# Performance work log

Hardware: AMD Instinct MI355X
Metric: run time of the kernel (lower is better)

Reference implementation:

```python
import jax, jax.numpy as jnp
import numpy as np

L, B, S, D, H, DH, F, W = 4, 4, 1024, 768, 12, 64, 3072, 128
R = 2 * W + 1  # 257 relative positions
EPS = 1e-8


def setup_inputs() -> dict:
    key = jax.random.key(0)
    ks = jax.random.split(key, 12)
    sc = 0.02
    rn = lambda k, shape: (jax.random.normal(k, shape, jnp.float32) * sc)
    return {
        'hidden_states': jax.random.normal(ks[0], (B, S, D), jnp.float32),
        'workspace_states': jax.random.normal(ks[1], (B, 8, D), jnp.float32),
        'attention_mask': jnp.ones((B, S), dtype=bool),
        'wq': rn(ks[2], (L, D, D)),
        'wk': rn(ks[3], (L, D, D)),
        'wv': rn(ks[4], (L, D, D)),
        'pos_q': rn(ks[5], (L, H, DH, R)),
        'pos_k': rn(ks[6], (L, H, DH, R)),
        'wo': rn(ks[7], (L, D, D)),
        'bo': jnp.zeros((L, D), jnp.float32),
        'w1': rn(ks[8], (L, D, F)),
        'b1': jnp.zeros((L, F), jnp.float32),
        'w2': rn(ks[9], (L, F, D)),
        'b2': jnp.zeros((L, D), jnp.float32),
        'ln_g': jnp.ones((L, D), jnp.float32),
        'ln_b': jnp.zeros((L, D), jnp.float32),
    }


def _encoder(hidden_states, workspace_states, attention_mask,
             wq, wk, wv, pos_q, pos_k, wo, bo, w1, b1, w2, b2, ln_g, ln_b):
    mask = attention_mask.astype(bool)
    ii = jnp.arange(S)[:, None]
    jj = jnp.arange(S)[None, :]
    # index = clamp(-(i-j) + w, 0, 2w)  -> relative-position bucket per (i,j)
    rel = jnp.clip(jj - ii + W, 0, 2 * W)            # [S,S] int
    band = jnp.abs(ii - jj) <= W                      # triu(-w) & ~triu(w+1)
    m = band[None, None] & mask[:, None, None, :] & mask[:, None, :, None]
    neg = jnp.finfo(jnp.float32).min
    h = hidden_states
    for l in range(L):
        q = (h @ wq[l]).reshape(B, S, H, DH).transpose(0, 2, 1, 3)  # [B,H,S,d]
        k = (h @ wk[l]).reshape(B, S, H, DH).transpose(0, 2, 1, 3)
        v = (h @ wv[l]).reshape(B, S, H, DH).transpose(0, 2, 1, 3)
        score = jnp.einsum('bhid,bhjd->bhij', q, k)
        qpk = jnp.einsum('bhid,hdr->bhir', q, pos_k[l])  # content-to-position
        kpq = jnp.einsum('bhjd,hdr->bhjr', k, pos_q[l])  # position-to-content
        c2p = qpk[:, :, ii, rel]                          # gather -> [B,H,S,S]
        p2c = jnp.swapaxes(kpq[:, :, ii, rel], -1, -2)    # gather + transpose
        score = score + c2p + p2c + neg * (~m)
        proba = jax.nn.softmax(score, axis=-1)
        ctx = jnp.einsum('bhij,bhjd->bhid', proba, v)
        ctx = ctx.transpose(0, 2, 1, 3).reshape(B, S, D)
        h = h + ctx @ wo[l] + bo[l]
        # shared workspace unit: pass-through (zero hidden update)
        inter = jax.nn.gelu(h @ w1[l] + b1[l], approximate=False)
        h = h + inter @ w2[l] + b2[l]
        mu = jnp.mean(h, axis=-1, keepdims=True)
        var = jnp.var(h, axis=-1, keepdims=True)
        h = (h - mu) / jnp.sqrt(var + EPS) * ln_g[l] + ln_b[l]
    return h


def reference(hidden_states, workspace_states, attention_mask,
              wq, wk, wv, pos_q, pos_k, wo, bo, w1, b1, w2, b2, ln_g, ln_b):
    return _encoder(hidden_states, workspace_states, attention_mask,
                    wq, wk, wv, pos_q, pos_k, wo, bo, w1, b1, w2, b2, ln_g, ln_b)
```

## Files before the change

### kernel.cpp

```cpp
#include <hip/hip_runtime.h>
#include <cstdint>
#include <cstddef>

#define L_ 4
#define B_ 4
#define S_ 1024
#define D_ 768
#define H_ 12
#define DH_ 64
#define F_ 3072
#define W_ 128
#define R_ 257
#define RP2_ 272
#define PTR_ 384

using f32x4 = __attribute__((ext_vector_type(4))) float;
typedef __bf16 bf16x8 __attribute__((ext_vector_type(8)));

__device__ __forceinline__ float bf2f(ushort u) {
  union { uint32_t i; float f; } x; x.i = ((uint32_t)u) << 16; return x.f;
}
__device__ __forceinline__ ushort f2bf(float f) {
  union { float f; uint32_t i; } x; x.f = f;
  uint32_t r = x.i + 0x7FFFu + ((x.i >> 16) & 1u);
  return (ushort)(r >> 16);
}

__global__ __launch_bounds__(256)
void transpose_cvt(const float* __restrict__ in, ushort* __restrict__ out,
                   int K, int N)
{
  __shared__ float tile[32][33];
  int n0 = blockIdx.x * 32, k0 = blockIdx.y * 32;
  int tx = threadIdx.x & 31, ty = threadIdx.x >> 5;
  #pragma unroll
  for (int r = 0; r < 32; r += 8)
    tile[ty + r][tx] = in[(size_t)(k0 + ty + r) * N + n0 + tx];
  __syncthreads();
  #pragma unroll
  for (int r = 0; r < 32; r += 8)
    out[(size_t)(n0 + ty + r) * K + k0 + tx] = f2bf(tile[tx][ty + r]);
}

__global__ __launch_bounds__(256)
void pos_transpose(const float* __restrict__ pos, ushort* __restrict__ posT)
{
  __shared__ float tile[32][33];
  int lh = blockIdx.x;
  int rt = blockIdx.y;
  int dt = blockIdx.z;
  int tx = threadIdx.x & 31, ty = threadIdx.x >> 5;
  const float* src = pos + (size_t)lh * 64 * R_;
  #pragma unroll
  for (int rr = 0; rr < 32; rr += 8) {
    int d = dt * 32 + ty + rr, r = rt * 32 + tx;
    tile[ty + rr][tx] = (r < R_) ? src[(size_t)d * R_ + r] : 0.f;
  }
  __syncthreads();
  ushort* dst = posT + (size_t)lh * PTR_ * 64;
  #pragma unroll
  for (int rr = 0; rr < 32; rr += 8) {
    int r = rt * 32 + ty + rr, d = dt * 32 + tx;
    dst[(size_t)r * 64 + d] = f2bf(tile[tx][ty + rr]);
  }
}

__global__ __launch_bounds__(256)
void init_h(const float* __restrict__ in, float* __restrict__ h,
            ushort* __restrict__ hbf, int n)
{
  int idx = blockIdx.x * 256 + threadIdx.x;
  if (idx < n) { float v = in[idx]; h[idx] = v; hbf[idx] = f2bf(v); }
}

__global__ __launch_bounds__(256)
void copy_out(const float* __restrict__ h, float* __restrict__ out, int n)
{
  int idx = blockIdx.x * 256 + threadIdx.x;
  if (idx < n) out[idx] = h[idx];
}

template<int EPI>
__global__ __launch_bounds__(256)
void gemm_bt(const ushort* __restrict__ A, const ushort* __restrict__ Bt,
             int M, int N, int K, const float* __restrict__ bias,
             float* __restrict__ resid, ushort* __restrict__ outbf)
{
  constexpr int KP = 56;
  __shared__ ushort Asm[128 * KP];
  __shared__ ushort Bsm[128 * KP];
  const int bm = blockIdx.x, bn = blockIdx.y;
  const int tid = threadIdx.x;
  const int lane = tid & 63, wave = tid >> 6;
  const int wm = wave >> 1, wn = wave & 1;
  const int srow = tid >> 2, scol = (tid & 3) * 8;
  const size_t rowA0 = (size_t)bm * 128, rowB0 = (size_t)bn * 128;
  const int fr = lane & 15;
  const int kb = (lane >> 4) * 8;

  f32x4 acc[4][4] = {};

  for (int k0 = 0; k0 < K; k0 += 32) {
    __syncthreads();
    #pragma unroll
    for (int it = 0; it < 2; ++it) {
      int r = srow + it * 64;
      *(uint4*)(&Asm[r * KP + scol]) =
          *(const uint4*)(A + (rowA0 + r) * K + k0 + scol);
      *(uint4*)(&Bsm[r * KP + scol]) =
          *(const uint4*)(Bt + (rowB0 + r) * K + k0 + scol);
    }
    __syncthreads();
    bf16x8 af[4], bfr[4];
    #pragma unroll
    for (int m = 0; m < 4; ++m)
      af[m] = *(const bf16x8*)(&Asm[(wm * 64 + m * 16 + fr) * KP + kb]);
    #pragma unroll
    for (int n = 0; n < 4; ++n)
      bfr[n] = *(const bf16x8*)(&Bsm[(wn * 64 + n * 16 + fr) * KP + kb]);
    #pragma unroll
    for (int m = 0; m < 4; ++m)
      #pragma unroll
      for (int n = 0; n < 4; ++n)
        acc[m][n] = __builtin_amdgcn_mfma_f32_16x16x32_bf16(
            af[m], bfr[n], acc[m][n], 0, 0, 0);
  }

  const int cr = (lane >> 4) * 4, cc = lane & 15;
  #pragma unroll
  for (int m = 0; m < 4; ++m) {
    #pragma unroll
    for (int n = 0; n < 4; ++n) {
      #pragma unroll
      for (int q = 0; q < 4; ++q) {
        size_t row = rowA0 + wm * 64 + m * 16 + cr + q;
        size_t col = rowB0 + wn * 64 + n * 16 + cc;
        float v = acc[m][n][q];
        if constexpr (EPI == 0) {
          outbf[row * N + col] = f2bf(v);
        } else if constexpr (EPI == 1) {
          float x = v + bias[col];
          float g = 0.5f * x * (1.0f + erff(x * 0.70710678118654752f));
          outbf[row * N + col] = f2bf(g);
        } else if constexpr (EPI == 2) {
          float x = v + bias[col] + resid[row * N + col];
          resid[row * N + col] = x;
          outbf[row * N + col] = f2bf(x);
        } else {
          float x = v + bias[col] + resid[row * N + col];
          resid[row * N + col] = x;
        }
      }
    }
  }
}

__global__ __launch_bounds__(256)
void pos_mfma(const ushort* __restrict__ qkv,
              const ushort* __restrict__ posTq, const ushort* __restrict__ posTk,
              ushort* __restrict__ qpk, ushort* __restrict__ kpq)
{
  __shared__ ushort Asm[128 * 64];
  __shared__ ushort Bsm[128 * 64];
  const int bm = blockIdx.x, bn = blockIdx.y, z = blockIdx.z;
  const int h = z >> 1, which = z & 1;
  const ushort* A  = qkv + (which ? 768 : 0) + h * 64;
  const ushort* Bt = (which ? posTq : posTk) + (size_t)h * PTR_ * 64;
  ushort* out = which ? kpq : qpk;
  const int tid = threadIdx.x, lane = tid & 63, w = tid >> 6;
  const int wm = w >> 1, wn = w & 1;
  const int c = lane & 15, g = lane >> 4;

  #pragma unroll
  for (int it = 0; it < 4; ++it) {
    int row = (tid >> 3) + it * 32;
    int d0 = (tid & 7) * 8;
    uint4 av = *(const uint4*)(A + (size_t)(bm * 128 + row) * 2304 + d0);
    *(uint4*)((char*)Asm + row * 128 + ((d0 * 2) ^ ((row & 7) << 4))) = av;
    uint4 bv = *(const uint4*)(Bt + (size_t)(bn * 128 + row) * 64 + d0);
    *(uint4*)((char*)Bsm + row * 128 + ((d0 * 2) ^ ((row & 7) << 4))) = bv;
  }
  __syncthreads();

  f32x4 acc[4][4] = {};
  #pragma unroll
  for (int ks = 0; ks < 2; ++ks) {
    bf16x8 af[4], bfr[4];
    #pragma unroll
    for (int m = 0; m < 4; ++m) {
      int row = wm * 64 + m * 16 + c;
      af[m] = *(const bf16x8*)((const char*)Asm + row * 128 +
                               ((ks * 64 + g * 16) ^ ((row & 7) << 4)));
    }
    #pragma unroll
    for (int n = 0; n < 4; ++n) {
      int row = wn * 64 + n * 16 + c;
      bfr[n] = *(const bf16x8*)((const char*)Bsm + row * 128 +
                                ((ks * 64 + g * 16) ^ ((row & 7) << 4)));
    }
    #pragma unroll
    for (int m = 0; m < 4; ++m)
      #pragma unroll
      for (int n = 0; n < 4; ++n)
        acc[m][n] = __builtin_amdgcn_mfma_f32_16x16x32_bf16(
            af[m], bfr[n], acc[m][n], 0, 0, 0);
  }

  #pragma unroll
  for (int m = 0; m < 4; ++m) {
    #pragma unroll
    for (int n = 0; n < 4; ++n) {
      #pragma unroll
      for (int q = 0; q < 4; ++q) {
        int rowl = wm * 64 + m * 16 + g * 4 + q;
        int bi = bm * 128 + rowl;
        int b = bi >> 10, i = bi & 1023;
        int col = bn * 128 + wn * 64 + n * 16 + c;
        if (col < RP2_)
          out[((size_t)((b * H_ + h) * S_ + i)) * RP2_ + col] =
              f2bf(acc[m][n][q]);
      }
    }
  }
}

__global__ __launch_bounds__(256)
void attn_mfma(const ushort* __restrict__ qkv,
               const ushort* __restrict__ qpk,
               const ushort* __restrict__ kpq,
               ushort* __restrict__ ctx)
{
  __shared__ ushort Qs[64 * 64];
  __shared__ ushort Ks[64 * 64];
  __shared__ ushort VTs[64 * 64];
  __shared__ ushort Ps[4][16 * 64];

  const int it0 = blockIdx.x;
  const int bh = blockIdx.y;
  const int b = bh / H_, h = bh - b * H_;
  const int i0 = it0 * 64;
  const int tid = threadIdx.x;
  const int lane = tid & 63, w = tid >> 6;
  const int c = lane & 15, g = lane >> 4;
  const size_t qkv_row0 = (size_t)(b * S_) * 2304;

  {
    int rr = tid >> 3, d0 = (tid & 7) * 8;
    #pragma unroll
    for (int it = 0; it < 2; ++it) {
      int row = rr + it * 32;
      uint4 v = *(const uint4*)(qkv + qkv_row0 + (size_t)(i0 + row) * 2304 +
                                h * 64 + d0);
      *(uint4*)((char*)Qs + row * 128 + ((d0 * 2) ^ ((row & 7) << 4))) = v;
    }
  }
  __syncthreads();

  bf16x8 qb[2];
  #pragma unroll
  for (int ks = 0; ks < 2; ++ks) {
    int row = w * 16 + c;
    qb[ks] = *(const bf16x8*)((const char*)Qs + row * 128 +
                              ((ks * 64 + g * 16) ^ ((row & 7) << 4)));
  }

  f32x4 acc[4] = {};
  float mrun = -1e30f, lrun = 0.f;
  const int i_mine = i0 + w * 16 + c;
  const ushort* qrow = qpk + ((size_t)(bh * S_) + i_mine) * RP2_;
  const ushort* kbase = kpq + (size_t)(bh * S_) * RP2_;

  for (int ccnk = 0; ccnk < 5; ++ccnk) {
    int jb = i0 - 128 + 64 * ccnk;
    if (jb < 0 || jb >= S_) continue;
    __syncthreads();
    {
      int rr = tid >> 3, d0 = (tid & 7) * 8;
      #pragma unroll
      for (int it = 0; it < 2; ++it) {
        int row = rr + it * 32;
        const ushort* src = qkv + qkv_row0 + (size_t)(jb + row) * 2304 +
                            768 + h * 64 + d0;
        uint4 kv = *(const uint4*)src;
        *(uint4*)((char*)Ks + row * 128 + ((d0 * 2) ^ ((row & 7) << 4))) = kv;
        uint4 vv = *(const uint4*)(src + 768);
        ushort tmp[8];
        *(uint4*)tmp = vv;
        #pragma unroll
        for (int e = 0; e < 8; ++e) {
          int e2 = (e + tid) & 7;
          int d = d0 + e2;
          *(ushort*)((char*)VTs + d * 128 + ((row * 2) ^ ((d & 7) << 4))) =
              tmp[e2];
        }
      }
    }
    __syncthreads();

    f32x4 sc[4];
    #pragma unroll
    for (int f = 0; f < 4; ++f) {
      f32x4 zz = {0.f, 0.f, 0.f, 0.f};
      #pragma unroll
      for (int ks = 0; ks < 2; ++ks) {
        int row = f * 16 + c;
        bf16x8 a = *(const bf16x8*)((const char*)Ks + row * 128 +
                                    ((ks * 64 + g * 16) ^ ((row & 7) << 4)));
        zz = __builtin_amdgcn_mfma_f32_16x16x32_bf16(a, qb[ks], zz, 0, 0, 0);
      }
      sc[f] = zz;
    }

    float svals[16];
    #pragma unroll
    for (int f = 0; f < 4; ++f) {
      #pragma unroll
      for (int q = 0; q < 4; ++q) {
        int jl = f * 16 + g * 4 + q;
        int j = jb + jl;
        int dlt = j - i_mine;
        float s = sc[f][q];
        if (dlt >= -W_ && dlt <= W_) {
          s += bf2f(qrow[dlt + W_]);
          s += bf2f(kbase[(size_t)j * RP2_ + (W_ - dlt)]);
        } else {
          s = -1e30f;
        }
        svals[f * 4 + q] = s;
      }
    }

    float cm = svals[0];
    #pragma unroll
    for (int q = 1; q < 16; ++q) cm = fmaxf(cm, svals[q]);
    cm = fmaxf(cm, __shfl_xor(cm, 16, 64));
    cm = fmaxf(cm, __shfl_xor(cm, 32, 64));
    float mnew = fmaxf(mrun, cm);
    float cf = __expf(mrun - mnew);
    float psum = 0.f;
    ushort pb[16];
    #pragma unroll
    for (int q = 0; q < 16; ++q) {
      float p = __expf(svals[q] - mnew);
      psum += p;
      pb[q] = f2bf(p);
    }
    psum += __shfl_xor(psum, 16, 64);
    psum += __shfl_xor(psum, 32, 64);
    lrun = lrun * cf + psum;
    mrun = mnew;

    float cfr[4];
    #pragma unroll
    for (int q = 0; q < 4; ++q) cfr[q] = __shfl(cf, (g << 2) + q, 64);
    #pragma unroll
    for (int n = 0; n < 4; ++n)
      #pragma unroll
      for (int q = 0; q < 4; ++q) acc[n][q] *= cfr[q];

    #pragma unroll
    for (int f = 0; f < 4; ++f) {
      uint2 p2;
      p2.x = (uint)pb[f * 4 + 0] | ((uint)pb[f * 4 + 1] << 16);
      p2.y = (uint)pb[f * 4 + 2] | ((uint)pb[f * 4 + 3] << 16);
      *(uint2*)((char*)&Ps[w][0] + c * 128 +
                ((f * 32 + g * 8) ^ ((c & 7) << 4))) = p2;
    }
    asm volatile("s_waitcnt lgkmcnt(0)" ::: "memory");

    #pragma unroll
    for (int ks = 0; ks < 2; ++ks) {
      bf16x8 pa = *(const bf16x8*)((const char*)&Ps[w][0] + c * 128 +
                                   ((ks * 64 + g * 16) ^ ((c & 7) << 4)));
      #pragma unroll
      for (int n = 0; n < 4; ++n) {
        int dd = n * 16 + c;
        bf16x8 bv = *(const bf16x8*)((const char*)VTs + dd * 128 +
                                     ((ks * 64 + g * 16) ^ ((dd & 7) << 4)));
        acc[n] = __builtin_amdgcn_mfma_f32_16x16x32_bf16(pa, bv, acc[n], 0, 0, 0);
      }
    }
  }

  float inv = 1.0f / lrun;
  float invr[4];
  #pragma unroll
  for (int q = 0; q < 4; ++q) invr[q] = __shfl(inv, (g << 2) + q, 64);
  #pragma unroll
  for (int n = 0; n < 4; ++n) {
    #pragma unroll
    for (int q = 0; q < 4; ++q) {
      int i_g = i0 + w * 16 + g * 4 + q;
      int d = n * 16 + c;
      ctx[((size_t)(b * S_ + i_g)) * D_ + h * 64 + d] = f2bf(acc[n][q] * invr[q]);
    }
  }
}

__global__ __launch_bounds__(256)
void ln_kernel(float* __restrict__ h, ushort* __restrict__ hbf,
               const float* __restrict__ g, const float* __restrict__ be)
{
  __shared__ float red[8];
  __shared__ float mv[2];
  int row = blockIdx.x, tid = threadIdx.x;
  float* hr = h + (size_t)row * D_;
  float v0 = hr[tid], v1 = hr[tid + 256], v2 = hr[tid + 512];
  float s = v0 + v1 + v2;
  float s2 = v0 * v0 + v1 * v1 + v2 * v2;
  #pragma unroll
  for (int o = 32; o >= 1; o >>= 1) {
    s += __shfl_xor(s, o, 64);
    s2 += __shfl_xor(s2, o, 64);
  }
  int wave = tid >> 6, lane = tid & 63;
  if (lane == 0) { red[wave] = s; red[4 + wave] = s2; }
  __syncthreads();
  if (tid == 0) {
    float ts = red[0] + red[1] + red[2] + red[3];
    float t2 = red[4] + red[5] + red[6] + red[7];
    float mu = ts / (float)D_;
    float var = t2 / (float)D_ - mu * mu;
    mv[0] = mu; mv[1] = rsqrtf(var + 1e-8f);
  }
  __syncthreads();
  float mu = mv[0], rstd = mv[1];
  #pragma unroll
  for (int cidx = 0; cidx < 3; ++cidx) {
    int col = tid + cidx * 256;
    float v = (cidx == 0) ? v0 : (cidx == 1) ? v1 : v2;
    float x = (v - mu) * rstd * g[col] + be[col];
    hr[col] = x;
    hbf[(size_t)row * D_ + col] = f2bf(x);
  }
}

extern "C" void kernel_launch(void* const* d_in, const int* in_sizes, int n_in,
                              void* d_out, int out_size, void* d_ws, size_t ws_size,
                              hipStream_t stream)
{
  const float* hidden = (const float*)d_in[0];
  const float* wq  = (const float*)d_in[3];
  const float* wk  = (const float*)d_in[4];
  const float* wv  = (const float*)d_in[5];
  const float* pq  = (const float*)d_in[6];
  const float* pk  = (const float*)d_in[7];
  const float* wo  = (const float*)d_in[8];
  const float* bo  = (const float*)d_in[9];
  const float* w1  = (const float*)d_in[10];
  const float* b1  = (const float*)d_in[11];
  const float* w2  = (const float*)d_in[12];
  const float* b2  = (const float*)d_in[13];
  const float* lng = (const float*)d_in[14];
  const float* lnb = (const float*)d_in[15];
  float* out = (float*)d_out;

  char* ws = (char*)d_ws;
  size_t off = 0;
  auto alloc = [&](size_t bytes) {
    void* p = ws + off;
    off += (bytes + 255) & ~(size_t)255;
    return p;
  };
  const size_t NT = (size_t)B_ * S_;
  ushort* wqkv_t = (ushort*)alloc((size_t)L_ * 2304 * 768 * 2);
  ushort* wo_t   = (ushort*)alloc((size_t)L_ * 768 * 768 * 2);
  ushort* w1_t   = (ushort*)alloc((size_t)L_ * 3072 * 768 * 2);
  ushort* w2_t   = (ushort*)alloc((size_t)L_ * 768 * 3072 * 2);
  ushort* posTq  = (ushort*)alloc((size_t)L_ * H_ * PTR_ * 64 * 2);
  ushort* posTk  = (ushort*)alloc((size_t)L_ * H_ * PTR_ * 64 * 2);
  float*  hbuf   = (float*) alloc(NT * D_ * 4);
  ushort* hbf    = (ushort*)alloc(NT * D_ * 2);
  ushort* qkv    = (ushort*)alloc(NT * 2304 * 2);
  ushort* qpk    = (ushort*)alloc((size_t)B_ * H_ * S_ * RP2_ * 2);
  ushort* kpq    = (ushort*)alloc((size_t)B_ * H_ * S_ * RP2_ * 2);
  ushort* ctx    = (ushort*)alloc(NT * D_ * 2);
  ushort* inter  = (ushort*)alloc(NT * F_ * 2);
  (void)ws_size; (void)in_sizes; (void)n_in; (void)out_size;

  for (int l = 0; l < L_; ++l) {
    const size_t dd = (size_t)768 * 768;
    transpose_cvt<<<dim3(24, 24), 256, 0, stream>>>(
        wq + l * dd, wqkv_t + (size_t)l * 2304 * 768, 768, 768);
    transpose_cvt<<<dim3(24, 24), 256, 0, stream>>>(
        wk + l * dd, wqkv_t + (size_t)l * 2304 * 768 + dd, 768, 768);
    transpose_cvt<<<dim3(24, 24), 256, 0, stream>>>(
        wv + l * dd, wqkv_t + (size_t)l * 2304 * 768 + 2 * dd, 768, 768);
    transpose_cvt<<<dim3(24, 24), 256, 0, stream>>>(
        wo + l * dd, wo_t + l * dd, 768, 768);
    transpose_cvt<<<dim3(96, 24), 256, 0, stream>>>(
        w1 + (size_t)l * 768 * 3072, w1_t + (size_t)l * 3072 * 768, 768, 3072);
    transpose_cvt<<<dim3(24, 96), 256, 0, stream>>>(
        w2 + (size_t)l * 3072 * 768, w2_t + (size_t)l * 768 * 3072, 3072, 768);
  }
  pos_transpose<<<dim3(48, 12, 2), 256, 0, stream>>>(pq, posTq);
  pos_transpose<<<dim3(48, 12, 2), 256, 0, stream>>>(pk, posTk);

  init_h<<<(int)((NT * D_ + 255) / 256), 256, 0, stream>>>(
      hidden, hbuf, hbf, (int)(NT * D_));

  for (int l = 0; l < L_; ++l) {
    gemm_bt<0><<<dim3(32, 18), 256, 0, stream>>>(
        hbf, wqkv_t + (size_t)l * 2304 * 768, 4096, 2304, 768,
        nullptr, nullptr, qkv);
    pos_mfma<<<dim3(32, 3, 24), 256, 0, stream>>>(
        qkv, posTq + (size_t)l * H_ * PTR_ * 64,
        posTk + (size_t)l * H_ * PTR_ * 64, qpk, kpq);
    attn_mfma<<<dim3(16, 48), 256, 0, stream>>>(qkv, qpk, kpq, ctx);
    gemm_bt<2><<<dim3(32, 6), 256, 0, stream>>>(
        ctx, wo_t + (size_t)l * 768 * 768, 4096, 768, 768,
        bo + l * 768, hbuf, hbf);
    gemm_bt<1><<<dim3(32, 24), 256, 0, stream>>>(
        hbf, w1_t + (size_t)l * 3072 * 768, 4096, 3072, 768,
        b1 + l * 3072, nullptr, inter);
    gemm_bt<3><<<dim3(32, 6), 256, 0, stream>>>(
        inter, w2_t + (size_t)l * 768 * 3072, 4096, 768, 3072,
        b2 + l * 768, hbuf, nullptr);
    ln_kernel<<<4096, 256, 0, stream>>>(hbuf, hbf, lng + l * 768, lnb + l * 768);
  }

  copy_out<<<(int)((NT * D_ + 255) / 256), 256, 0, stream>>>(
      hbuf, out, (int)(NT * D_));
}
```

Baseline: 1.271 ms.

## Use direct global-to-LDS loads with XOR swizzle and BK=64 in GEMM

The bf16 GEMM now stages A and B tiles with global_load_lds, which writes global memory straight into LDS without a register round-trip. The K tile doubles to 64, halving the number of barrier pairs per output tile. An XOR swizzle on the 16-byte chunk index replaces the padded LDS layout to avoid bank conflicts. It is still single-buffered, so loads and MFMA work do not overlap, and it depends on the per-lane LDS address pattern of the builtin being correct.

```diff
diff --git a/kernel.cpp b/kernel.cpp
--- a/kernel.cpp
+++ b/kernel.cpp
@@ -17,6 +17,9 @@
 using f32x4 = __attribute__((ext_vector_type(4))) float;
 typedef __bf16 bf16x8 __attribute__((ext_vector_type(8)));
 
+#define AS1(p) ((const __attribute__((address_space(1))) void*)(p))
+#define AS3(p) ((__attribute__((address_space(3))) void*)(p))
+
 __device__ __forceinline__ float bf2f(ushort u) {
   union { uint32_t i; float f; } x; x.i = ((uint32_t)u) << 16; return x.f;
 }
@@ -86,47 +89,60 @@
              int M, int N, int K, const float* __restrict__ bias,
              float* __restrict__ resid, ushort* __restrict__ outbf)
 {
-  constexpr int KP = 56;
-  __shared__ ushort Asm[128 * KP];
-  __shared__ ushort Bsm[128 * KP];
+  __shared__ ushort Asm[128 * 64];
+  __shared__ ushort Bsm[128 * 64];
   const int bm = blockIdx.x, bn = blockIdx.y;
   const int tid = threadIdx.x;
-  const int lane = tid & 63, wave = tid >> 6;
-  const int wm = wave >> 1, wn = wave & 1;
-  const int srow = tid >> 2, scol = (tid & 3) * 8;
+  const int lane = tid & 63, w = tid >> 6;
+  const int wm = w >> 1, wn = w & 1;
+  const int c = lane & 15, g = lane >> 4;
   const size_t rowA0 = (size_t)bm * 128, rowB0 = (size_t)bn * 128;
-  const int fr = lane & 15;
-  const int kb = (lane >> 4) * 8;
+
+  const int sr  = lane >> 3;
+  const int sc8 = ((lane & 7) ^ sr) * 8;
+  const ushort* aSrc = A  + (rowA0 + w * 32 + sr) * (size_t)K + sc8;
+  const ushort* bSrc = Bt + (rowB0 + w * 32 + sr) * (size_t)K + sc8;
+  const ushort* aDst = Asm + (w * 32) * 64;
+  const ushort* bDst = Bsm + (w * 32) * 64;
 
   f32x4 acc[4][4] = {};
 
-  for (int k0 = 0; k0 < K; k0 += 32) {
+  for (int k0 = 0; k0 < K; k0 += 64) {
     __syncthreads();
     #pragma unroll
-    for (int it = 0; it < 2; ++it) {
-      int r = srow + it * 64;
-      *(uint4*)(&Asm[r * KP + scol]) =
-          *(const uint4*)(A + (rowA0 + r) * K + k0 + scol);
-      *(uint4*)(&Bsm[r * KP + scol]) =
-          *(const uint4*)(Bt + (rowB0 + r) * K + k0 + scol);
+    for (int it = 0; it < 4; ++it) {
+      __builtin_amdgcn_global_load_lds(AS1(aSrc + (size_t)(it * 8) * K + k0),
+                                       AS3(aDst + it * 8 * 64), 16, 0, 0);
+      __builtin_amdgcn_global_load_lds(AS1(bSrc + (size_t)(it * 8) * K + k0),
+                                       AS3(bDst + it * 8 * 64), 16, 0, 0);
     }
     __syncthreads();
-    bf16x8 af[4], bfr[4];
-    #pragma unroll
-    for (int m = 0; m < 4; ++m)
-      af[m] = *(const bf16x8*)(&Asm[(wm * 64 + m * 16 + fr) * KP + kb]);
-    #pragma unroll
-    for (int n = 0; n < 4; ++n)
-      bfr[n] = *(const bf16x8*)(&Bsm[(wn * 64 + n * 16 + fr) * KP + kb]);
-    #pragma unroll
-    for (int m = 0; m < 4; ++m)
-      #pragma unroll
-      for (int n = 0; n < 4; ++n)
-        acc[m][n] = __builtin_amdgcn_mfma_f32_16x16x32_bf16(
-            af[m], bfr[n], acc[m][n], 0, 0, 0);
-  }
-
-  const int cr = (lane >> 4) * 4, cc = lane & 15;
+
+    #pragma unroll
+    for (int ks = 0; ks < 2; ++ks) {
+      bf16x8 af[4], bfr[4];
+      #pragma unroll
+      for (int m = 0; m < 4; ++m) {
+        int row = wm * 64 + m * 16 + c;
+        af[m] = *(const bf16x8*)((const char*)Asm + row * 128 +
+                                 ((ks * 64 + g * 16) ^ ((row & 7) << 4)));
+      }
+      #pragma unroll
+      for (int n = 0; n < 4; ++n) {
+        int row = wn * 64 + n * 16 + c;
+        bfr[n] = *(const bf16x8*)((const char*)Bsm + row * 128 +
+                                  ((ks * 64 + g * 16) ^ ((row & 7) << 4)));
+      }
+      #pragma unroll
+      for (int m = 0; m < 4; ++m)
+        #pragma unroll
+        for (int n = 0; n < 4; ++n)
+          acc[m][n] = __builtin_amdgcn_mfma_f32_16x16x32_bf16(
+              af[m], bfr[n], acc[m][n], 0, 0, 0);
+    }
+  }
+
+  const int cr = g * 4, cc = c;
   #pragma unroll
   for (int m = 0; m < 4; ++m) {
     #pragma unroll
@@ -140,8 +156,8 @@
           outbf[row * N + col] = f2bf(v);
         } else if constexpr (EPI == 1) {
           float x = v + bias[col];
-          float g = 0.5f * x * (1.0f + erff(x * 0.70710678118654752f));
-          outbf[row * N + col] = f2bf(g);
+          float gl = 0.5f * x * (1.0f + erff(x * 0.70710678118654752f));
+          outbf[row * N + col] = f2bf(gl);
         } else if constexpr (EPI == 2) {
           float x = v + bias[col] + resid[row * N + col];
           resid[row * N + col] = x;
```

Result: faster. 1.162 ms (-8.6%).
